# Kernel optimization log

Measured on AMD Instinct MI355X. Metric: run time of the kernel, lower is better.

Reference implementation:

```python
import jax, jax.numpy as jnp
import numpy as np

D = 512
H = 4
DK = D // H
N_ACTOR = 4096
N_BV = 4096
NEG = jnp.float32(-1e9)  # stands in for -inf; exp underflows to exactly 0 in fp32


def setup_inputs() -> dict:
    key = jax.random.key(0)
    k1, k2, k3, k4, k5, k6, k7, k8 = jax.random.split(key, 8)
    a_z = jax.random.normal(k1, (N_ACTOR, D), dtype=jnp.float32)
    bv_z = jax.random.normal(k2, (N_BV, D), dtype=jnp.float32)
    mask = jax.random.uniform(k3, (N_ACTOR, N_BV)) > 0.5
    weight = jax.random.normal(k4, (N_ACTOR, N_BV), dtype=jnp.float32)
    # nn.MultiheadAttention parameters (packed in_proj, out_proj)
    in_proj_w = jax.random.normal(k5, (3 * D, D), dtype=jnp.float32) * 0.02
    in_proj_b = jax.random.normal(k6, (3 * D,), dtype=jnp.float32) * 0.02
    out_w = jax.random.normal(k7, (D, D), dtype=jnp.float32) * 0.02
    out_b = jax.random.normal(k8, (D,), dtype=jnp.float32) * 0.02
    return {"a_z": a_z, "bv_z": bv_z, "mask": mask, "weight": weight,
            "in_proj_w": in_proj_w, "in_proj_b": in_proj_b,
            "out_w": out_w, "out_b": out_b}


def reference(a_z, bv_z, mask, weight, in_proj_w, in_proj_b, out_w, out_b):
    n, d = a_z.shape
    m = bv_z.shape[0]
    a = jnp.nan_to_num(a_z, nan=0.0, posinf=1.0, neginf=-1.0)
    kv = jnp.nan_to_num(bv_z, nan=0.0, posinf=1.0, neginf=-1.0)
    w = jnp.nan_to_num(weight, nan=0.0, posinf=1.0, neginf=-1.0)
    mf = mask.astype(a.dtype)
    valid = jnp.any(mask, axis=1)  # actors with at least one unmasked key

    # attn_mask = weight masked with -inf at padded keys (covers key_padding_mask too)
    bias = jnp.where(mask, w, NEG)  # [n, m]

    wq, wk, wv = jnp.split(in_proj_w, 3, axis=0)
    bq, bk, bv = jnp.split(in_proj_b, 3, axis=0)
    q = ((a @ wq.T + bq).reshape(n, H, DK)) * (1.0 / np.sqrt(DK))
    k = (kv @ wk.T + bk).reshape(m, H, DK)
    v = (kv @ wv.T + bv).reshape(m, H, DK)

    scores = jnp.einsum('nhd,mhd->nhm', q, k) + bias[:, None, :]
    attn = jax.nn.softmax(scores, axis=-1)                  # [n, h, m]
    ctx = jnp.einsum('nhm,mhd->nhd', attn, v).reshape(n, d)
    out = ctx @ out_w.T + out_b                              # out_proj

    # topic alignment: mean over head-chunks of the projected output
    topic = out.reshape(n, H, DK).mean(axis=1)               # [n, dk]

    # influence: softmax-normalized weight scores dotted with avg attn weights
    aw = attn.mean(axis=1) * mf                              # head-averaged attn, masked
    norm_scores = jax.nn.softmax(bias, axis=-1) * mf
    influence = jnp.sum(norm_scores * aw, axis=-1)           # [n]

    # actors with no valid key are scattered back as zeros
    topic = jnp.where(valid[:, None], topic, 0.0)
    influence = jnp.where(valid, influence, 0.0)
    return topic, influence
```

## Files before the change

### kernel.cpp

```cpp
#include <hip/hip_runtime.h>
#include <hip/hip_bf16.h>
#include <cstdint>
#include <cstddef>


typedef __attribute__((ext_vector_type(8))) short bf16x8;
typedef __attribute__((ext_vector_type(4))) short bf16x4;
typedef __attribute__((ext_vector_type(4))) float f32x4;

#define MFMA32(a, b, c) __builtin_amdgcn_mfma_f32_16x16x32_bf16((a), (b), (c), 0, 0, 0)
#define MFMA16(a, b, c) __builtin_amdgcn_mfma_f32_16x16x16bf16_1k((a), (b), (c), 0, 0, 0)

static __device__ __forceinline__ short f2b(float x) {
  union { float f; unsigned u; } v; v.f = x;
  unsigned r = v.u + 0x7fffu + ((v.u >> 16) & 1u);
  return (short)(r >> 16);
}

__global__ __launch_bounds__(256) void k_qkv(
    const float* __restrict__ a, const float* __restrict__ kv,
    const float* __restrict__ w, const float* __restrict__ bias,
    short* __restrict__ Qb, short* __restrict__ Kp, short* __restrict__ Vp)
{
  __shared__ short As[128 * 40];
  __shared__ short Bs[64 * 40];
  const int blk = blockIdx.x;
  const int bm = blk % 32, bn = blk / 32;
  const int m0 = bm * 128, n0 = bn * 64;
  const float* __restrict__ Ain = (bn < 8) ? a : kv;
  const int tid = threadIdx.x;
  const int lane = tid & 63, wvi = tid >> 6;
  const int wm = (wvi >> 1) * 64, wn = (wvi & 1) * 32;
  const int c = lane & 15, g = lane >> 4;
  const int srA = tid >> 1, scA = (tid & 1) * 16;
  const int srB = tid >> 2, scB = (tid & 3) * 8;

  f32x4 acc[4][2];
#pragma unroll
  for (int i = 0; i < 4; ++i)
#pragma unroll
    for (int j = 0; j < 2; ++j) acc[i][j] = (f32x4)0.f;

  for (int k0 = 0; k0 < 512; k0 += 32) {
    const float* ap = Ain + (size_t)(m0 + srA) * 512 + k0 + scA;
#pragma unroll
    for (int j = 0; j < 4; ++j) {
      f32x4 av = *(const f32x4*)(ap + 4 * j);
      bf16x4 as;
      as.x = f2b(av.x); as.y = f2b(av.y); as.z = f2b(av.z); as.w = f2b(av.w);
      *(bf16x4*)(&As[srA * 40 + scA + 4 * j]) = as;
    }
    const float* bp = w + (size_t)(n0 + srB) * 512 + k0 + scB;
#pragma unroll
    for (int j = 0; j < 2; ++j) {
      f32x4 bv = *(const f32x4*)(bp + 4 * j);
      bf16x4 bs;
      bs.x = f2b(bv.x); bs.y = f2b(bv.y); bs.z = f2b(bv.z); bs.w = f2b(bv.w);
      *(bf16x4*)(&Bs[srB * 40 + scB + 4 * j]) = bs;
    }
    __syncthreads();
    bf16x8 af[4], bfg[2];
#pragma unroll
    for (int t = 0; t < 4; ++t)
      af[t] = *(const bf16x8*)(&As[(wm + t * 16 + c) * 40 + g * 8]);
#pragma unroll
    for (int t = 0; t < 2; ++t)
      bfg[t] = *(const bf16x8*)(&Bs[(wn + t * 16 + c) * 40 + g * 8]);
#pragma unroll
    for (int rt = 0; rt < 4; ++rt)
#pragma unroll
      for (int ct = 0; ct < 2; ++ct)
        acc[rt][ct] = MFMA32(af[rt], bfg[ct], acc[rt][ct]);
    __syncthreads();
  }

#pragma unroll
  for (int ct = 0; ct < 2; ++ct) {
    const int col = n0 + wn + ct * 16 + c;
    const float bj = bias[col];
#pragma unroll
    for (int rt = 0; rt < 4; ++rt) {
      const int row = m0 + wm + rt * 16 + g * 4;
      const int mc = row >> 4;
      if (col < 512) {
#pragma unroll
        for (int r = 0; r < 4; ++r)
          Qb[(size_t)(row + r) * 512 + col] = f2b((acc[rt][ct][r] + bj) * 0.08838834764831843f);
      } else if (col < 1024) {
        const int colK = col - 512;
        const int h = colK >> 7, dk = colK & 127;
        const int ks = dk >> 5, gk = (dk >> 3) & 3, j = dk & 7;
        short* base = Kp + (size_t)((((h * 256 + mc) * 4 + ks) * 64) + gk * 16 + g * 4) * 8 + j;
#pragma unroll
        for (int r = 0; r < 4; ++r) base[r * 8] = f2b(acc[rt][ct][r] + bj);
      } else {
        const int colV = col - 1024;
        const int h = colV >> 7, db = (colV & 127) >> 4, cv = colV & 15;
        bf16x4 pk;
#pragma unroll
        for (int r = 0; r < 4; ++r) pk[r] = f2b(acc[rt][ct][r] + bj);
        *(bf16x4*)(Vp + (size_t)((((h * 256 + mc) * 8 + db) * 64) + g * 16 + cv) * 4) = pk;
      }
    }
  }
}

__global__ __launch_bounds__(256, 4) void k_attn(
    const short* __restrict__ Qb, const short* __restrict__ Kp,
    const short* __restrict__ Vp, const float* __restrict__ wgt,
    const int* __restrict__ msk, const int S,
    short* __restrict__ Opart, float* __restrict__ lpart,
    float* __restrict__ cipart, float* __restrict__ lbpart)
{
  const int bx = blockIdx.x;
  const int rb = bx & 255, sp = bx >> 8;
  const int n0 = rb * 16;
  const int mlen = 4096 / S;
  const int mc0 = (sp * mlen) >> 4;
  const int nch = mlen >> 4;
  const int tid = threadIdx.x;
  const int lane = tid & 63, h = tid >> 6;
  const int c = lane & 15, g = lane >> 4;

  bf16x8 qf[4];
#pragma unroll
  for (int ks = 0; ks < 4; ++ks)
    qf[ks] = *(const bf16x8*)(Qb + (size_t)(n0 + c) * 512 + h * 128 + ks * 32 + g * 8);

  f32x4 O[8];
#pragma unroll
  for (int db = 0; db < 8; ++db) O[db] = (f32x4)0.f;
  float lh = 0.f, lb = 0.f, ci = 0.f;

  const short* Kw = Kp + (size_t)h * 524288 + (size_t)lane * 8 + (size_t)mc0 * 2048;
  const short* Vw = Vp + (size_t)h * 524288 + (size_t)lane * 4 + (size_t)mc0 * 2048;
  const int* mbase_p = msk + (size_t)(n0 + c) * 4096 + g * 4 + (size_t)mc0 * 16;
  const float* wbase_p = wgt + (size_t)(n0 + c) * 4096 + g * 4 + (size_t)mc0 * 16;

  int4 mkN = *(const int4*)(mbase_p);
  f32x4 wvN = *(const f32x4*)(wbase_p);

  for (int t = 0; t < nch; ++t) {
    bf16x8 kf[4];
#pragma unroll
    for (int ks = 0; ks < 4; ++ks)
      kf[ks] = *(const bf16x8*)(Kw + t * 2048 + ks * 512);
    bf16x4 vf[8];
#pragma unroll
    for (int db = 0; db < 8; ++db)
      vf[db] = *(const bf16x4*)(Vw + t * 2048 + db * 256);

    const int4 mkC = mkN;
    const f32x4 wvC = wvN;
    const int tn = (t + 1 < nch) ? (t + 1) : t;
    mkN = *(const int4*)(mbase_p + tn * 16);
    wvN = *(const f32x4*)(wbase_p + tn * 16);

    f32x4 Sv = (f32x4)0.f;
#pragma unroll
    for (int ks = 0; ks < 4; ++ks) Sv = MFMA32(kf[ks], qf[ks], Sv);
    const float e0 = mkC.x ? __expf(wvC.x) : 0.f;
    const float e1 = mkC.y ? __expf(wvC.y) : 0.f;
    const float e2 = mkC.z ? __expf(wvC.z) : 0.f;
    const float e3 = mkC.w ? __expf(wvC.w) : 0.f;
    const float p0 = __expf(Sv[0]) * e0, p1 = __expf(Sv[1]) * e1;
    const float p2 = __expf(Sv[2]) * e2, p3 = __expf(Sv[3]) * e3;
    lh += (p0 + p1) + (p2 + p3);
    lb += (e0 + e1) + (e2 + e3);
    ci += (p0 * e0 + p1 * e1) + (p2 * e2 + p3 * e3);
    bf16x4 pa;
    pa[0] = f2b(p0); pa[1] = f2b(p1); pa[2] = f2b(p2); pa[3] = f2b(p3);
#pragma unroll
    for (int db = 0; db < 8; ++db)
      O[db] = MFMA16(pa, vf[db], O[db]);
  }

  lh += __shfl_xor(lh, 16, 64); lh += __shfl_xor(lh, 32, 64);
  lb += __shfl_xor(lb, 16, 64); lb += __shfl_xor(lb, 32, 64);
  ci += __shfl_xor(ci, 16, 64); ci += __shfl_xor(ci, 32, 64);

  float inv[4];
#pragma unroll
  for (int r = 0; r < 4; ++r)
    inv[r] = 1.f / fmaxf(__shfl(lh, 4 * g + r, 64), 1e-30f);
#pragma unroll
  for (int db = 0; db < 8; ++db)
#pragma unroll
    for (int r = 0; r < 4; ++r)
      Opart[(size_t)sp * (4096 * 512) + (size_t)(n0 + g * 4 + r) * 512 +
            h * 128 + db * 16 + c] = f2b(O[db][r] * inv[r]);

  if (g == 0) {
    const int row = n0 + c;
    lpart[((size_t)sp * 4 + h) * 4096 + row] = lh;
    cipart[((size_t)sp * 4 + h) * 4096 + row] = ci;
    if (h == 0) lbpart[(size_t)sp * 4096 + row] = lb;
  }
}

__global__ __launch_bounds__(256) void k_comb(
    const short* __restrict__ Opart, const float* __restrict__ lpart,
    const float* __restrict__ cipart, const float* __restrict__ lbpart,
    const int S, short* __restrict__ ctxb, float* __restrict__ validw,
    float* __restrict__ infl)
{
  const int tid = threadIdx.x;
  const int rloc = tid >> 5, cseg = tid & 31;
  const int row = blockIdx.x * 8 + rloc;
  const int col0 = cseg * 16;
  const int h = col0 >> 7;

  float l[4], ciS[4], lb = 0.f;
#pragma unroll
  for (int hh = 0; hh < 4; ++hh) { l[hh] = 0.f; ciS[hh] = 0.f; }
  for (int s = 0; s < S; ++s) {
#pragma unroll
    for (int hh = 0; hh < 4; ++hh) {
      l[hh]   += lpart[((size_t)s * 4 + hh) * 4096 + row];
      ciS[hh] += cipart[((size_t)s * 4 + hh) * 4096 + row];
    }
    lb += lbpart[(size_t)s * 4096 + row];
  }

  float acc[16];
#pragma unroll
  for (int j = 0; j < 16; ++j) acc[j] = 0.f;
  const float linv = 1.f / fmaxf(l[h], 1e-30f);
  for (int s = 0; s < S; ++s) {
    const float w_s = lpart[((size_t)s * 4 + h) * 4096 + row] * linv;
    const bf16x8 o0 = *(const bf16x8*)(Opart + (size_t)s * (4096 * 512) + (size_t)row * 512 + col0);
    const bf16x8 o1 = *(const bf16x8*)(Opart + (size_t)s * (4096 * 512) + (size_t)row * 512 + col0 + 8);
#pragma unroll
    for (int j = 0; j < 8; ++j) {
      union { unsigned u; float f; } v0, v1;
      v0.u = ((unsigned)(unsigned short)o0[j]) << 16;
      v1.u = ((unsigned)(unsigned short)o1[j]) << 16;
      acc[j]     += w_s * v0.f;
      acc[8 + j] += w_s * v1.f;
    }
  }
  bf16x8 c0, c1;
#pragma unroll
  for (int j = 0; j < 8; ++j) { c0[j] = f2b(acc[j]); c1[j] = f2b(acc[8 + j]); }
  *(bf16x8*)(ctxb + (size_t)row * 512 + col0) = c0;
  *(bf16x8*)(ctxb + (size_t)row * 512 + col0 + 8) = c1;

  if (cseg == 0) {
    validw[row] = (lb > 0.f) ? 1.f : 0.f;
    float s_ = 0.f;
#pragma unroll
    for (int hh = 0; hh < 4; ++hh) s_ += ciS[hh] / fmaxf(l[hh], 1e-30f);
    infl[row] = (lb > 0.f) ? s_ / (4.f * lb) : 0.f;
  }
}

__global__ void k_fold(const float* __restrict__ ow, const float* __restrict__ ob,
                       short* __restrict__ Wf, float* __restrict__ bfo)
{
  const int idx = blockIdx.x * 256 + threadIdx.x;
  if (idx < 128 * 512) {
    const int dk = idx >> 9, d = idx & 511;
    const float s = 0.25f * (ow[(size_t)dk * 512 + d] + ow[(size_t)(dk + 128) * 512 + d] +
                             ow[(size_t)(dk + 256) * 512 + d] + ow[(size_t)(dk + 384) * 512 + d]);
    Wf[(size_t)dk * 512 + d] = f2b(s);
  }
  if (idx < 128) bfo[idx] = 0.25f * (ob[idx] + ob[idx + 128] + ob[idx + 256] + ob[idx + 384]);
}

__global__ __launch_bounds__(256) void k_out(
    const short* __restrict__ ctxb, const short* __restrict__ Wf,
    const float* __restrict__ bfo, const float* __restrict__ validw,
    float* __restrict__ topic)
{
  const int tid = threadIdx.x;
  const int lane = tid & 63, wvi = tid >> 6;
  const int m0 = blockIdx.x * 16;
  const int c = lane & 15, g = lane >> 4;

  f32x4 acc[2];
  acc[0] = (f32x4)0.f; acc[1] = (f32x4)0.f;

  for (int k0 = 0; k0 < 512; k0 += 32) {
    const bf16x8 af = *(const bf16x8*)(ctxb + (size_t)(m0 + c) * 512 + k0 + g * 8);
#pragma unroll
    for (int dbl = 0; dbl < 2; ++dbl) {
      const bf16x8 bfr = *(const bf16x8*)(Wf + (size_t)(wvi * 32 + dbl * 16 + c) * 512 + k0 + g * 8);
      acc[dbl] = MFMA32(af, bfr, acc[dbl]);
    }
  }

#pragma unroll
  for (int r = 0; r < 4; ++r) {
    const int row = m0 + g * 4 + r;
    const float va = validw[row];
#pragma unroll
    for (int dbl = 0; dbl < 2; ++dbl) {
      const int col = wvi * 32 + dbl * 16 + c;
      const float vl = (va > 0.5f) ? (acc[dbl][r] + bfo[col]) : 0.f;
      topic[(size_t)row * 128 + col] = vl;
    }
  }
}

extern "C" void kernel_launch(void* const* d_in, const int* in_sizes, int n_in,
                              void* d_out, int out_size, void* d_ws, size_t ws_size,
                              hipStream_t stream) {
  const float* a_z  = (const float*)d_in[0];
  const float* bv_z = (const float*)d_in[1];
  const int*   mask = (const int*)d_in[2];
  const float* wgt  = (const float*)d_in[3];
  const float* ipw  = (const float*)d_in[4];
  const float* ipb  = (const float*)d_in[5];
  const float* ow   = (const float*)d_in[6];
  const float* ob   = (const float*)d_in[7];
  float* topic = (float*)d_out;
  float* infl  = (float*)d_out + 4096 * 128;

  const size_t MB = (size_t)1 << 20;
  char* ws = (char*)d_ws;
  short* Qb     = (short*)(ws);
  short* Kp     = (short*)(ws + 4 * MB);
  short* Vp     = (short*)(ws + 8 * MB);
  short* ctxb   = (short*)(ws + 12 * MB);
  float* validw = (float*)(ws + 16 * MB);
  short* Wf     = (short*)(ws + 16 * MB + (64 << 10));
  float* bfo    = (float*)(ws + 16 * MB + (224 << 10));
  const size_t pbase0 = 16 * MB + (256 << 10);

  auto need = [&](int S) { return pbase0 + (size_t)S * (4 * MB + (144 << 10)); };
  int S = 8;
  while (S > 1 && need(S) > ws_size) S >>= 1;

  char* pbase = ws + pbase0;
  short* Opart  = (short*)(pbase);
  float* lpart  = (float*)(pbase + (size_t)S * 4 * MB);
  float* cipart = (float*)(pbase + (size_t)S * 4 * MB + ((size_t)S << 16));
  float* lbpart = (float*)(pbase + (size_t)S * 4 * MB + ((size_t)S << 17));

  k_qkv <<<768, 256, 0, stream>>>(a_z, bv_z, ipw, ipb, Qb, Kp, Vp);
  k_fold<<<256, 256, 0, stream>>>(ow, ob, Wf, bfo);
  k_attn<<<256 * S, 256, 0, stream>>>(Qb, Kp, Vp, wgt, mask, S, Opart, lpart, cipart, lbpart);
  k_comb<<<512, 256, 0, stream>>>(Opart, lpart, cipart, lbpart, S, ctxb, validw, infl);
  k_out <<<256, 256, 0, stream>>>(ctxb, Wf, bfo, validw, topic);
}
```

Before: 354.7 us.

## Process two 16-row query blocks per attention workgroup to reuse K/V loads

```diff
diff --git a/kernel.cpp b/kernel.cpp
--- a/kernel.cpp
+++ b/kernel.cpp
@@ -105,7 +105,7 @@
   }
 }
 
-__global__ __launch_bounds__(256, 4) void k_attn(
+__global__ __launch_bounds__(256, 3) void k_attn(
     const short* __restrict__ Qb, const short* __restrict__ Kp,
     const short* __restrict__ Vp, const float* __restrict__ wgt,
     const int* __restrict__ msk, const int S,
@@ -113,8 +113,8 @@
     float* __restrict__ cipart, float* __restrict__ lbpart)
 {
   const int bx = blockIdx.x;
-  const int rb = bx & 255, sp = bx >> 8;
-  const int n0 = rb * 16;
+  const int rb = bx & 127, sp = bx >> 7;
+  const int n0 = rb * 32;
   const int mlen = 4096 / S;
   const int mc0 = (sp * mlen) >> 4;
   const int nch = mlen >> 4;
@@ -122,23 +122,30 @@
   const int lane = tid & 63, h = tid >> 6;
   const int c = lane & 15, g = lane >> 4;
 
-  bf16x8 qf[4];
-#pragma unroll
-  for (int ks = 0; ks < 4; ++ks)
-    qf[ks] = *(const bf16x8*)(Qb + (size_t)(n0 + c) * 512 + h * 128 + ks * 32 + g * 8);
-
-  f32x4 O[8];
-#pragma unroll
-  for (int db = 0; db < 8; ++db) O[db] = (f32x4)0.f;
-  float lh = 0.f, lb = 0.f, ci = 0.f;
+  bf16x8 qf[2][4];
+#pragma unroll
+  for (int nb = 0; nb < 2; ++nb)
+#pragma unroll
+    for (int ks = 0; ks < 4; ++ks)
+      qf[nb][ks] = *(const bf16x8*)(Qb + (size_t)(n0 + nb * 16 + c) * 512 + h * 128 + ks * 32 + g * 8);
+
+  f32x4 O[2][8];
+#pragma unroll
+  for (int nb = 0; nb < 2; ++nb)
+#pragma unroll
+    for (int db = 0; db < 8; ++db) O[nb][db] = (f32x4)0.f;
+  float lh[2] = {0.f, 0.f}, lb2[2] = {0.f, 0.f}, ci[2] = {0.f, 0.f};
 
   const short* Kw = Kp + (size_t)h * 524288 + (size_t)lane * 8 + (size_t)mc0 * 2048;
   const short* Vw = Vp + (size_t)h * 524288 + (size_t)lane * 4 + (size_t)mc0 * 2048;
-  const int* mbase_p = msk + (size_t)(n0 + c) * 4096 + g * 4 + (size_t)mc0 * 16;
-  const float* wbase_p = wgt + (size_t)(n0 + c) * 4096 + g * 4 + (size_t)mc0 * 16;
-
-  int4 mkN = *(const int4*)(mbase_p);
-  f32x4 wvN = *(const f32x4*)(wbase_p);
+  const int* mp = msk + (size_t)(n0 + c) * 4096 + g * 4 + (size_t)mc0 * 16;
+  const float* wp = wgt + (size_t)(n0 + c) * 4096 + g * 4 + (size_t)mc0 * 16;
+  const int nboff = 16 * 4096;
+
+  int4 mk0 = *(const int4*)(mp);
+  f32x4 wv0 = *(const f32x4*)(wp);
+  int4 mk1 = *(const int4*)(mp + nboff);
+  f32x4 wv1 = *(const f32x4*)(wp + nboff);
 
   for (int t = 0; t < nch; ++t) {
     bf16x8 kf[4];
@@ -150,51 +157,78 @@
     for (int db = 0; db < 8; ++db)
       vf[db] = *(const bf16x4*)(Vw + t * 2048 + db * 256);
 
-    const int4 mkC = mkN;
-    const f32x4 wvC = wvN;
+    const float ea0 = mk0.x ? __expf(wv0.x) : 0.f;
+    const float ea1 = mk0.y ? __expf(wv0.y) : 0.f;
+    const float ea2 = mk0.z ? __expf(wv0.z) : 0.f;
+    const float ea3 = mk0.w ? __expf(wv0.w) : 0.f;
+    const float eb0 = mk1.x ? __expf(wv1.x) : 0.f;
+    const float eb1 = mk1.y ? __expf(wv1.y) : 0.f;
+    const float eb2 = mk1.z ? __expf(wv1.z) : 0.f;
+    const float eb3 = mk1.w ? __expf(wv1.w) : 0.f;
+
     const int tn = (t + 1 < nch) ? (t + 1) : t;
-    mkN = *(const int4*)(mbase_p + tn * 16);
-    wvN = *(const f32x4*)(wbase_p + tn * 16);
-
-    f32x4 Sv = (f32x4)0.f;
-#pragma unroll
-    for (int ks = 0; ks < 4; ++ks) Sv = MFMA32(kf[ks], qf[ks], Sv);
-    const float e0 = mkC.x ? __expf(wvC.x) : 0.f;
-    const float e1 = mkC.y ? __expf(wvC.y) : 0.f;
-    const float e2 = mkC.z ? __expf(wvC.z) : 0.f;
-    const float e3 = mkC.w ? __expf(wvC.w) : 0.f;
-    const float p0 = __expf(Sv[0]) * e0, p1 = __expf(Sv[1]) * e1;
-    const float p2 = __expf(Sv[2]) * e2, p3 = __expf(Sv[3]) * e3;
-    lh += (p0 + p1) + (p2 + p3);
-    lb += (e0 + e1) + (e2 + e3);
-    ci += (p0 * e0 + p1 * e1) + (p2 * e2 + p3 * e3);
-    bf16x4 pa;
-    pa[0] = f2b(p0); pa[1] = f2b(p1); pa[2] = f2b(p2); pa[3] = f2b(p3);
+    mk0 = *(const int4*)(mp + tn * 16);
+    wv0 = *(const f32x4*)(wp + tn * 16);
+    mk1 = *(const int4*)(mp + nboff + tn * 16);
+    wv1 = *(const f32x4*)(wp + nboff + tn * 16);
+
+    f32x4 Sv0 = (f32x4)0.f, Sv1 = (f32x4)0.f;
+#pragma unroll
+    for (int ks = 0; ks < 4; ++ks) {
+      Sv0 = MFMA32(kf[ks], qf[0][ks], Sv0);
+      Sv1 = MFMA32(kf[ks], qf[1][ks], Sv1);
+    }
+
+    const float p00 = __expf(Sv0[0]) * ea0, p01 = __expf(Sv0[1]) * ea1;
+    const float p02 = __expf(Sv0[2]) * ea2, p03 = __expf(Sv0[3]) * ea3;
+    const float p10 = __expf(Sv1[0]) * eb0, p11 = __expf(Sv1[1]) * eb1;
+    const float p12 = __expf(Sv1[2]) * eb2, p13 = __expf(Sv1[3]) * eb3;
+    lh[0] += (p00 + p01) + (p02 + p03);
+    lh[1] += (p10 + p11) + (p12 + p13);
+    lb2[0] += (ea0 + ea1) + (ea2 + ea3);
+    lb2[1] += (eb0 + eb1) + (eb2 + eb3);
+    ci[0] += (p00 * ea0 + p01 * ea1) + (p02 * ea2 + p03 * ea3);
+    ci[1] += (p10 * eb0 + p11 * eb1) + (p12 * eb2 + p13 * eb3);
+    bf16x4 pa0, pa1;
+    pa0[0] = f2b(p00); pa0[1] = f2b(p01); pa0[2] = f2b(p02); pa0[3] = f2b(p03);
+    pa1[0] = f2b(p10); pa1[1] = f2b(p11); pa1[2] = f2b(p12); pa1[3] = f2b(p13);
+
+#pragma unroll
+    for (int db = 0; db < 8; ++db) {
+      O[0][db] = MFMA16(pa0, vf[db], O[0][db]);
+      O[1][db] = MFMA16(pa1, vf[db], O[1][db]);
+    }
+  }
+
+#pragma unroll
+  for (int nb = 0; nb < 2; ++nb) {
+    lh[nb] += __shfl_xor(lh[nb], 16, 64); lh[nb] += __shfl_xor(lh[nb], 32, 64);
+    lb2[nb] += __shfl_xor(lb2[nb], 16, 64); lb2[nb] += __shfl_xor(lb2[nb], 32, 64);
+    ci[nb] += __shfl_xor(ci[nb], 16, 64); ci[nb] += __shfl_xor(ci[nb], 32, 64);
+  }
+
+#pragma unroll
+  for (int nb = 0; nb < 2; ++nb) {
+    float inv[4];
+#pragma unroll
+    for (int r = 0; r < 4; ++r)
+      inv[r] = 1.f / fmaxf(__shfl(lh[nb], 4 * g + r, 64), 1e-30f);
 #pragma unroll
     for (int db = 0; db < 8; ++db)
-      O[db] = MFMA16(pa, vf[db], O[db]);
-  }
-
-  lh += __shfl_xor(lh, 16, 64); lh += __shfl_xor(lh, 32, 64);
-  lb += __shfl_xor(lb, 16, 64); lb += __shfl_xor(lb, 32, 64);
-  ci += __shfl_xor(ci, 16, 64); ci += __shfl_xor(ci, 32, 64);
-
-  float inv[4];
-#pragma unroll
-  for (int r = 0; r < 4; ++r)
-    inv[r] = 1.f / fmaxf(__shfl(lh, 4 * g + r, 64), 1e-30f);
-#pragma unroll
-  for (int db = 0; db < 8; ++db)
-#pragma unroll
-    for (int r = 0; r < 4; ++r)
-      Opart[(size_t)sp * (4096 * 512) + (size_t)(n0 + g * 4 + r) * 512 +
-            h * 128 + db * 16 + c] = f2b(O[db][r] * inv[r]);
+#pragma unroll
+      for (int r = 0; r < 4; ++r)
+        Opart[(size_t)sp * (4096 * 512) + (size_t)(n0 + nb * 16 + g * 4 + r) * 512 +
+              h * 128 + db * 16 + c] = f2b(O[nb][db][r] * inv[r]);
+  }
 
   if (g == 0) {
-    const int row = n0 + c;
-    lpart[((size_t)sp * 4 + h) * 4096 + row] = lh;
-    cipart[((size_t)sp * 4 + h) * 4096 + row] = ci;
-    if (h == 0) lbpart[(size_t)sp * 4096 + row] = lb;
+#pragma unroll
+    for (int nb = 0; nb < 2; ++nb) {
+      const int row = n0 + nb * 16 + c;
+      lpart[((size_t)sp * 4 + h) * 4096 + row] = lh[nb];
+      cipart[((size_t)sp * 4 + h) * 4096 + row] = ci[nb];
+      if (h == 0) lbpart[(size_t)sp * 4096 + row] = lb2[nb];
+    }
   }
 }
 
@@ -339,7 +373,7 @@
 
   k_qkv <<<768, 256, 0, stream>>>(a_z, bv_z, ipw, ipb, Qb, Kp, Vp);
   k_fold<<<256, 256, 0, stream>>>(ow, ob, Wf, bfo);
-  k_attn<<<256 * S, 256, 0, stream>>>(Qb, Kp, Vp, wgt, mask, S, Opart, lpart, cipart, lbpart);
+  k_attn<<<128 * S, 256, 0, stream>>>(Qb, Kp, Vp, wgt, mask, S, Opart, lpart, cipart, lbpart);
   k_comb<<<512, 256, 0, stream>>>(Opart, lpart, cipart, lbpart, S, ctxb, validw, infl);
   k_out <<<256, 256, 0, stream>>>(ctxb, Wf, bfo, validw, topic);
 }
```

New measurement: 356.8 us. About the same (+0.6%).
